# Kernel tuning notes

Hardware: AMD Instinct MI355X
Metric: run time of the kernel (lower is better)

The kernel has to match this reference:

```python
import jax, jax.numpy as jnp
import numpy as np

I, H, O = 3, 50, 1

def setup_inputs() -> dict:
    key = jax.random.key(0)
    ks = jax.random.split(key, 7)
    B, T = 4096, 512
    s_ih = 1.0 / np.sqrt(H)
    x = jax.random.normal(ks[0], (B, T, I), dtype=jnp.float32)
    W_ih = jax.random.uniform(ks[1], (3 * H, I), jnp.float32, -s_ih, s_ih)
    W_hh = jax.random.uniform(ks[2], (3 * H, H), jnp.float32, -s_ih, s_ih)
    b_ih = jax.random.uniform(ks[3], (3 * H,), jnp.float32, -s_ih, s_ih)
    b_hh = jax.random.uniform(ks[4], (3 * H,), jnp.float32, -s_ih, s_ih)
    W_fc = jax.random.uniform(ks[5], (O, H), jnp.float32, -s_ih, s_ih)
    b_fc = jax.random.uniform(ks[6], (O,), jnp.float32, -s_ih, s_ih)
    return {"x": x, "W_ih": W_ih, "W_hh": W_hh, "b_ih": b_ih, "b_hh": b_hh,
            "W_fc": W_fc, "b_fc": b_fc}

def _gru_last_hidden(x, W_ih, W_hh, b_ih, b_hh):
    # x: [B, T, I]. Precompute input projections for all timesteps (one big GEMM).
    B, T, _ = x.shape
    gi = jnp.einsum('bti,gi->btg', x, W_ih) + b_ih  # [B, T, 3H]
    gi = jnp.moveaxis(gi, 1, 0)  # [T, B, 3H] for scan over time

    W_hr, W_hz, W_hn = W_hh[:H], W_hh[H:2*H], W_hh[2*H:]
    b_hr, b_hz, b_hn = b_hh[:H], b_hh[H:2*H], b_hh[2*H:]

    def step(h, gi_t):
        gir, giz, gin = gi_t[:, :H], gi_t[:, H:2*H], gi_t[:, 2*H:]
        r = jax.nn.sigmoid(gir + h @ W_hr.T + b_hr)
        z = jax.nn.sigmoid(giz + h @ W_hz.T + b_hz)
        n = jnp.tanh(gin + r * (h @ W_hn.T + b_hn))
        h_new = (1.0 - z) * n + z * h
        return h_new, None

    h0 = jnp.zeros((B, H), dtype=x.dtype)
    h_last, _ = jax.lax.scan(step, h0, gi)
    return h_last  # [B, H]

def reference(x, W_ih, W_hh, b_ih, b_hh, W_fc, b_fc):
    h_last = _gru_last_hidden(x, W_ih, W_hh, b_ih, b_hh)
    out = h_last @ W_fc.T + b_fc  # [B, 1]
    return out.squeeze(-1)  # [B]
```

## Files before the change

### kernel.cpp

```cpp
#include <hip/hip_runtime.h>
#include <hip/hip_bf16.h>

#define T_LEN 512
#define HID 50
#define NBATCH 4096

using short8  = __attribute__((ext_vector_type(8))) short;
using floatx4 = __attribute__((ext_vector_type(4))) float;

__device__ __forceinline__ float sigm(float v) {
  return __builtin_amdgcn_rcpf(1.0f + __builtin_amdgcn_exp2f(-1.442695041f * v));
}
__device__ __forceinline__ float tanh_f(float v) {
  return 1.0f - 2.0f * __builtin_amdgcn_rcpf(1.0f + __builtin_amdgcn_exp2f(2.885390082f * v));
}

__device__ __forceinline__ short8 afrag(const char* plane, int rowoff, int off16) {
  return *(const short8*)(plane + rowoff + off16);
}

__global__ __launch_bounds__(256, 1)
void gru_mfma_kernel(const float* __restrict__ x,
                     const float* __restrict__ W_ih,
                     const float* __restrict__ W_hh,
                     const float* __restrict__ b_ih,
                     const float* __restrict__ b_hh,
                     const float* __restrict__ W_fc,
                     const float* __restrict__ b_fc,
                     float* __restrict__ out) {
  __shared__ alignas(16) unsigned char lds[16384];
  char* xs   = (char*)lds;
  char* hbuf = (char*)lds + 12288;

  const int tid  = threadIdx.x;
  const int lane = tid & 63;
  const int w    = tid >> 6;
  const int ucol = lane & 15;
  const int kg   = (lane >> 4) & 3;
  const int b0   = blockIdx.x * 16;
  const int u    = 16 * w + ucol;
  const bool uv  = (u < HID);

  const float c_r  = uv ? (b_ih[u] + b_hh[u]) : 0.f;
  const float c_z  = uv ? (b_ih[50 + u] + b_hh[50 + u]) : 0.f;
  const float c_ni = uv ? b_ih[100 + u] : 0.f;
  const float c_nh = uv ? b_hh[100 + u] : 0.f;
  float u_r[3], u_z[3], u_n[3];
#pragma unroll
  for (int c = 0; c < 3; ++c) {
    u_r[c] = uv ? W_ih[u * 3 + c] : 0.f;
    u_z[c] = uv ? W_ih[(50 + u) * 3 + c] : 0.f;
    u_n[c] = uv ? W_ih[(100 + u) * 3 + c] : 0.f;
  }
  const float wfc = uv ? W_fc[u] : 0.f;

  short8 Bh[3][2];
#pragma unroll
  for (int g = 0; g < 3; ++g) {
    const int row = uv ? (g * 50 + u) : 0;
    const float* Wrow = W_hh + row * HID;
#pragma unroll
    for (int f = 0; f < 2; ++f) {
      union { short a[8]; short8 s; } ph;
#pragma unroll
      for (int e = 0; e < 8; ++e) {
        const int k = 32 * f + 8 * kg + e;
        const float v = (uv && k < HID) ? Wrow[k] : 0.f;
        __hip_bfloat16 bh = __float2bfloat16(v);
        ph.a[e] = *(short*)&bh;
      }
      Bh[g][f] = ph.s;
    }
  }

  ((float4*)hbuf)[tid] = make_float4(0.f, 0.f, 0.f, 0.f);

  float h[4] = {0.f, 0.f, 0.f, 0.f};

  const int arow = ucol * 128;
  const int axr  = (ucol & 7) << 4;
  const floatx4 z4 = {0.f, 0.f, 0.f, 0.f};

  for (int tc = 0; tc < 8; ++tc) {
    {
      const int sm = tid >> 4, seg = tid & 15;
      const float* xb = x + (size_t)(b0 + sm) * (T_LEN * 3) + tc * 192 + seg * 12;
      const float4 v0 = *(const float4*)(xb + 0);
      const float4 v1 = *(const float4*)(xb + 4);
      const float4 v2 = *(const float4*)(xb + 8);
      const float vv[12] = {v0.x, v0.y, v0.z, v0.w, v1.x, v1.y, v1.z, v1.w, v2.x, v2.y, v2.z, v2.w};
#pragma unroll
      for (int jj = 0; jj < 12; ++jj) {
        const int i = seg * 12 + jj;
        *(float*)(xs + (i / 3) * 192 + (i % 3) * 64 + sm * 4) = vv[jj];
      }
    }
    __syncthreads();

#pragma unroll 2
    for (int s = 0; s < 64; ++s) {
      const int par = s & 1;
      const char* rp = hbuf + par * 2048;
      char*       wp = hbuf + (par ^ 1) * 2048;

      const float4 xv0 = *(const float4*)(xs + s * 192 + 0 * 64 + kg * 16);
      const float4 xv1 = *(const float4*)(xs + s * 192 + 1 * 64 + kg * 16);
      const float4 xv2 = *(const float4*)(xs + s * 192 + 2 * 64 + kg * 16);

      const short8 A0 = afrag(rp, arow, (16 * kg +  0) ^ axr);
      const short8 A1 = afrag(rp, arow, (16 * kg + 64) ^ axr);

      floatx4 aR = __builtin_amdgcn_mfma_f32_16x16x32_bf16(A0, Bh[0][0], z4, 0, 0, 0);
      aR = __builtin_amdgcn_mfma_f32_16x16x32_bf16(A1, Bh[0][1], aR, 0, 0, 0);
      floatx4 aZ = __builtin_amdgcn_mfma_f32_16x16x32_bf16(A0, Bh[1][0], z4, 0, 0, 0);
      aZ = __builtin_amdgcn_mfma_f32_16x16x32_bf16(A1, Bh[1][1], aZ, 0, 0, 0);
      floatx4 aN = __builtin_amdgcn_mfma_f32_16x16x32_bf16(A0, Bh[2][0], z4, 0, 0, 0);
      aN = __builtin_amdgcn_mfma_f32_16x16x32_bf16(A1, Bh[2][1], aN, 0, 0, 0);

      const float xa[4]  = {xv0.x, xv0.y, xv0.z, xv0.w};
      const float xb_[4] = {xv1.x, xv1.y, xv1.z, xv1.w};
      const float xc[4]  = {xv2.x, xv2.y, xv2.z, xv2.w};
#pragma unroll
      for (int r = 0; r < 4; ++r) {
        const float x0 = xa[r], x1 = xb_[r], x2 = xc[r];
        const float gr = fmaf(x0, u_r[0], fmaf(x1, u_r[1], fmaf(x2, u_r[2], c_r)));
        const float gz = fmaf(x0, u_z[0], fmaf(x1, u_z[1], fmaf(x2, u_z[2], c_z)));
        const float gn = fmaf(x0, u_n[0], fmaf(x1, u_n[1], fmaf(x2, u_n[2], c_ni)));
        const float rr = sigm(aR[r] + gr);
        const float zz = sigm(aZ[r] + gz);
        const float nv = gn + rr * (aN[r] + c_nh);
        const float nn = tanh_f(nv);
        const float hn = nn + zz * (h[r] - nn);
        h[r] = hn;
        __hip_bfloat16 bh = __float2bfloat16(hn);
        const int mrow = 4 * kg + r;
        *(unsigned short*)(wp + mrow * 128 + ((2 * u) ^ ((mrow & 7) << 4))) =
            *(const unsigned short*)&bh;
      }
      __syncthreads();
    }
  }

  float p[4];
#pragma unroll
  for (int r = 0; r < 4; ++r) p[r] = h[r] * wfc;
#pragma unroll
  for (int mask = 1; mask < 16; mask <<= 1) {
#pragma unroll
    for (int r = 0; r < 4; ++r) p[r] += __shfl_xor(p[r], mask);
  }
  if (ucol == 0) {
    *(float4*)(lds + (w * 16 + 4 * kg) * 4) = make_float4(p[0], p[1], p[2], p[3]);
  }
  __syncthreads();
  if (tid < 16) {
    float ssum = 0.f;
#pragma unroll
    for (int ww = 0; ww < 4; ++ww) ssum += *(const float*)(lds + (ww * 16 + tid) * 4);
    out[b0 + tid] = ssum + b_fc[0];
  }
}

extern "C" void kernel_launch(void* const* d_in, const int* in_sizes, int n_in,
                              void* d_out, int out_size, void* d_ws, size_t ws_size,
                              hipStream_t stream) {
  const float* x    = (const float*)d_in[0];
  const float* W_ih = (const float*)d_in[1];
  const float* W_hh = (const float*)d_in[2];
  const float* b_ih = (const float*)d_in[3];
  const float* b_hh = (const float*)d_in[4];
  const float* W_fc = (const float*)d_in[5];
  const float* b_fc = (const float*)d_in[6];
  float* out = (float*)d_out;

  dim3 grid(NBATCH / 16);
  dim3 block(256);
  gru_mfma_kernel<<<grid, block, 0, stream>>>(x, W_ih, W_hh, b_ih, b_hh, W_fc, b_fc, out);
}
```

Measured before the change: 222.1 us.

## Transpose MFMA operands so each lane owns four hidden units of one sample

Swaps the A/B operands of the recurrent MFMAs so the weights become the A fragment and the hidden state the B fragment. Each lane's accumulator then holds four consecutive hidden units of a single batch row instead of four batch rows of one unit. The new hidden state is written to LDS as a single packed 64-bit store of four bf16 values rather than four scattered 16-bit stores. Only one x value per input channel is read per step, and the final reduction shrinks to two shuffles. In exchange each lane keeps per-unit bias and input-weight constants for four units, raising register use.

```diff
diff --git a/kernel.cpp b/kernel.cpp
--- a/kernel.cpp
+++ b/kernel.cpp
@@ -13,10 +13,6 @@
 }
 __device__ __forceinline__ float tanh_f(float v) {
   return 1.0f - 2.0f * __builtin_amdgcn_rcpf(1.0f + __builtin_amdgcn_exp2f(2.885390082f * v));
-}
-
-__device__ __forceinline__ short8 afrag(const char* plane, int rowoff, int off16) {
-  return *(const short8*)(plane + rowoff + off16);
 }
 
 __global__ __launch_bounds__(256, 1)
@@ -41,20 +37,26 @@
   const int u    = 16 * w + ucol;
   const bool uv  = (u < HID);
 
-  const float c_r  = uv ? (b_ih[u] + b_hh[u]) : 0.f;
-  const float c_z  = uv ? (b_ih[50 + u] + b_hh[50 + u]) : 0.f;
-  const float c_ni = uv ? b_ih[100 + u] : 0.f;
-  const float c_nh = uv ? b_hh[100 + u] : 0.f;
-  float u_r[3], u_z[3], u_n[3];
+  float c_r[4], c_z[4], c_ni[4], c_nh[4], wfc[4];
+  float ur[4][3], uz[4][3], un[4][3];
 #pragma unroll
-  for (int c = 0; c < 3; ++c) {
-    u_r[c] = uv ? W_ih[u * 3 + c] : 0.f;
-    u_z[c] = uv ? W_ih[(50 + u) * 3 + c] : 0.f;
-    u_n[c] = uv ? W_ih[(100 + u) * 3 + c] : 0.f;
+  for (int r = 0; r < 4; ++r) {
+    const int uu = 16 * w + 4 * kg + r;
+    const bool vr = (uu < HID);
+    c_r[r]  = vr ? (b_ih[uu] + b_hh[uu]) : 0.f;
+    c_z[r]  = vr ? (b_ih[50 + uu] + b_hh[50 + uu]) : 0.f;
+    c_ni[r] = vr ? b_ih[100 + uu] : 0.f;
+    c_nh[r] = vr ? b_hh[100 + uu] : 0.f;
+    wfc[r]  = vr ? W_fc[uu] : 0.f;
+#pragma unroll
+    for (int c = 0; c < 3; ++c) {
+      ur[r][c] = vr ? W_ih[uu * 3 + c] : 0.f;
+      uz[r][c] = vr ? W_ih[(50 + uu) * 3 + c] : 0.f;
+      un[r][c] = vr ? W_ih[(100 + uu) * 3 + c] : 0.f;
+    }
   }
-  const float wfc = uv ? W_fc[u] : 0.f;
 
-  short8 Bh[3][2];
+  short8 Wf[3][2];
 #pragma unroll
   for (int g = 0; g < 3; ++g) {
     const int row = uv ? (g * 50 + u) : 0;
@@ -69,7 +71,7 @@
         __hip_bfloat16 bh = __float2bfloat16(v);
         ph.a[e] = *(short*)&bh;
       }
-      Bh[g][f] = ph.s;
+      Wf[g][f] = ph.s;
     }
   }
 
@@ -77,8 +79,9 @@
 
   float h[4] = {0.f, 0.f, 0.f, 0.f};
 
-  const int arow = ucol * 128;
+  const int hrow = ucol * 128;
   const int axr  = (ucol & 7) << 4;
+  const int soff = hrow + ((32 * w + 8 * kg) ^ axr);
   const floatx4 z4 = {0.f, 0.f, 0.f, 0.f};
 
   for (int tc = 0; tc < 8; ++tc) {
@@ -103,54 +106,52 @@
       const char* rp = hbuf + par * 2048;
       char*       wp = hbuf + (par ^ 1) * 2048;
 
-      const float4 xv0 = *(const float4*)(xs + s * 192 + 0 * 64 + kg * 16);
-      const float4 xv1 = *(const float4*)(xs + s * 192 + 1 * 64 + kg * 16);
-      const float4 xv2 = *(const float4*)(xs + s * 192 + 2 * 64 + kg * 16);
+      const float x0 = *(const float*)(xs + s * 192 +   0 + ucol * 4);
+      const float x1 = *(const float*)(xs + s * 192 +  64 + ucol * 4);
+      const float x2 = *(const float*)(xs + s * 192 + 128 + ucol * 4);
 
-      const short8 A0 = afrag(rp, arow, (16 * kg +  0) ^ axr);
-      const short8 A1 = afrag(rp, arow, (16 * kg + 64) ^ axr);
+      const short8 H0 = *(const short8*)(rp + hrow + ((16 * kg)      ^ axr));
+      const short8 H1 = *(const short8*)(rp + hrow + ((16 * kg + 64) ^ axr));
 
-      floatx4 aR = __builtin_amdgcn_mfma_f32_16x16x32_bf16(A0, Bh[0][0], z4, 0, 0, 0);
-      aR = __builtin_amdgcn_mfma_f32_16x16x32_bf16(A1, Bh[0][1], aR, 0, 0, 0);
-      floatx4 aZ = __builtin_amdgcn_mfma_f32_16x16x32_bf16(A0, Bh[1][0], z4, 0, 0, 0);
-      aZ = __builtin_amdgcn_mfma_f32_16x16x32_bf16(A1, Bh[1][1], aZ, 0, 0, 0);
-      floatx4 aN = __builtin_amdgcn_mfma_f32_16x16x32_bf16(A0, Bh[2][0], z4, 0, 0, 0);
-      aN = __builtin_amdgcn_mfma_f32_16x16x32_bf16(A1, Bh[2][1], aN, 0, 0, 0);
+      floatx4 aR = __builtin_amdgcn_mfma_f32_16x16x32_bf16(Wf[0][0], H0, z4, 0, 0, 0);
+      aR = __builtin_amdgcn_mfma_f32_16x16x32_bf16(Wf[0][1], H1, aR, 0, 0, 0);
+      floatx4 aZ = __builtin_amdgcn_mfma_f32_16x16x32_bf16(Wf[1][0], H0, z4, 0, 0, 0);
+      aZ = __builtin_amdgcn_mfma_f32_16x16x32_bf16(Wf[1][1], H1, aZ, 0, 0, 0);
+      floatx4 aN = __builtin_amdgcn_mfma_f32_16x16x32_bf16(Wf[2][0], H0, z4, 0, 0, 0);
+      aN = __builtin_amdgcn_mfma_f32_16x16x32_bf16(Wf[2][1], H1, aN, 0, 0, 0);
 
-      const float xa[4]  = {xv0.x, xv0.y, xv0.z, xv0.w};
-      const float xb_[4] = {xv1.x, xv1.y, xv1.z, xv1.w};
-      const float xc[4]  = {xv2.x, xv2.y, xv2.z, xv2.w};
+      unsigned int hw[2];
 #pragma unroll
-      for (int r = 0; r < 4; ++r) {
-        const float x0 = xa[r], x1 = xb_[r], x2 = xc[r];
-        const float gr = fmaf(x0, u_r[0], fmaf(x1, u_r[1], fmaf(x2, u_r[2], c_r)));
-        const float gz = fmaf(x0, u_z[0], fmaf(x1, u_z[1], fmaf(x2, u_z[2], c_z)));
-        const float gn = fmaf(x0, u_n[0], fmaf(x1, u_n[1], fmaf(x2, u_n[2], c_ni)));
-        const float rr = sigm(aR[r] + gr);
-        const float zz = sigm(aZ[r] + gz);
-        const float nv = gn + rr * (aN[r] + c_nh);
-        const float nn = tanh_f(nv);
-        const float hn = nn + zz * (h[r] - nn);
-        h[r] = hn;
-        __hip_bfloat16 bh = __float2bfloat16(hn);
-        const int mrow = 4 * kg + r;
-        *(unsigned short*)(wp + mrow * 128 + ((2 * u) ^ ((mrow & 7) << 4))) =
-            *(const unsigned short*)&bh;
+      for (int q = 0; q < 2; ++q) {
+        unsigned int pk = 0;
+#pragma unroll
+        for (int j = 0; j < 2; ++j) {
+          const int r = 2 * q + j;
+          const float gr = fmaf(x0, ur[r][0], fmaf(x1, ur[r][1], fmaf(x2, ur[r][2], c_r[r])));
+          const float gz = fmaf(x0, uz[r][0], fmaf(x1, uz[r][1], fmaf(x2, uz[r][2], c_z[r])));
+          const float gn = fmaf(x0, un[r][0], fmaf(x1, un[r][1], fmaf(x2, un[r][2], c_ni[r])));
+          const float rr = sigm(aR[r] + gr);
+          const float zz = sigm(aZ[r] + gz);
+          const float omz = 1.0f - zz;
+          const float zh  = zz * h[r];
+          const float nn  = tanh_f(gn + rr * (aN[r] + c_nh[r]));
+          h[r] = fmaf(nn, omz, zh);
+          __hip_bfloat16 bh = __float2bfloat16(h[r]);
+          pk |= (unsigned int)(*(const unsigned short*)&bh) << (16 * j);
+        }
+        hw[q] = pk;
       }
+      *(unsigned long long*)(wp + soff) =
+          (unsigned long long)hw[0] | ((unsigned long long)hw[1] << 32);
       __syncthreads();
     }
   }
 
-  float p[4];
-#pragma unroll
-  for (int r = 0; r < 4; ++r) p[r] = h[r] * wfc;
-#pragma unroll
-  for (int mask = 1; mask < 16; mask <<= 1) {
-#pragma unroll
-    for (int r = 0; r < 4; ++r) p[r] += __shfl_xor(p[r], mask);
-  }
-  if (ucol == 0) {
-    *(float4*)(lds + (w * 16 + 4 * kg) * 4) = make_float4(p[0], p[1], p[2], p[3]);
+  float p = h[0] * wfc[0] + h[1] * wfc[1] + h[2] * wfc[2] + h[3] * wfc[3];
+  p += __shfl_xor(p, 16);
+  p += __shfl_xor(p, 32);
+  if (lane < 16) {
+    *(float*)(lds + (w * 16 + ucol) * 4) = p;
   }
   __syncthreads();
   if (tid < 16) {
```

Result: faster. 216.6 us (median of 2 runs) (-2.5%).
